# Kernel tuning notes

Hardware: AMD Instinct MI355X
Metric: run time of the kernel (lower is better)

Reference implementation:

```python
import jax, jax.numpy as jnp
import numpy as np

N_NODES = 100000
N_EDGES = 1600000
IN_DIM = 64
OUT_DIM = 64


def setup_inputs() -> dict:
    key = jax.random.key(0)
    k1, k2, k3, k4, k5, k6 = jax.random.split(key, 6)
    # xavier-uniform-ish scales for the linear weights (gain=1.414)
    fc_bound = 1.414 * np.sqrt(6.0 / (IN_DIM + OUT_DIM))
    at_bound = 1.414 * np.sqrt(6.0 / (OUT_DIM + 1))
    return {
        "h_src": jax.random.normal(k1, (N_NODES, IN_DIM), dtype=jnp.float32),
        "h_dst": jax.random.normal(k2, (N_NODES, IN_DIM), dtype=jnp.float32),
        "W_fc": jax.random.uniform(k3, (OUT_DIM, IN_DIM), dtype=jnp.float32,
                                   minval=-fc_bound, maxval=fc_bound),
        "w_attn": jax.random.uniform(k4, (OUT_DIM,), dtype=jnp.float32,
                                     minval=-at_bound, maxval=at_bound),
        "src": jax.random.randint(k5, (N_EDGES,), 0, N_NODES, dtype=jnp.int64),
        "dst": jnp.sort(jax.random.randint(k6, (N_EDGES,), 0, N_NODES, dtype=jnp.int64)),
    }


def reference(h_src, h_dst, W_fc, w_attn, src, dst):
    # Per-edge feature difference: dst - src  (edge_attention)
    diff_e = h_dst[dst] - h_src[src]                      # [E, in_dim]
    # fc projection (dropout p=0 in eval) then attention score
    d = diff_e @ W_fc.T                                   # [E, out_dim]
    e = jnp.tanh(d @ w_attn)                              # [E]
    # Segment softmax over incoming edges of each destination node
    m = jax.ops.segment_max(e, dst, num_segments=N_NODES)  # [N], -inf for empty
    ex = jnp.exp(e - m[dst])                              # [E]
    s = jax.ops.segment_sum(ex, dst, num_segments=N_NODES)  # [N]
    alpha = ex / s[dst]                                   # [E]
    # Weighted sum aggregation of projected diffs per destination node
    h_diff = jax.ops.segment_sum(alpha[:, None] * d, dst, num_segments=N_NODES)  # [N, out_dim]
    return jax.nn.elu(h_diff)
```

## Files before the change

kernel.cpp:

```cpp
#include <hip/hip_runtime.h>
#include <hip/hip_fp16.h>
#include <math.h>

#define NN 100000
#define NE 1600000
#define DIM 64
#define HST 72

typedef __attribute__((ext_vector_type(8))) __fp16 half8;
typedef __attribute__((ext_vector_type(4))) float f32x4;

__device__ __forceinline__ __half2 u2h2(unsigned u) { __half2 h; __builtin_memcpy(&h, &u, 4); return h; }
__device__ __forceinline__ unsigned h22u(__half2 h) { unsigned u; __builtin_memcpy(&u, &h, 4); return u; }
__device__ __forceinline__ unsigned pk_f16(float a, float b) {
    auto h = __builtin_amdgcn_cvt_pkrtz(a, b);
    unsigned u; __builtin_memcpy(&u, &h, 4); return u;
}

__global__ __launch_bounds__(256) void proj_kernel(
    const float* __restrict__ h_src, const float* __restrict__ h_dst,
    const float* __restrict__ W, const float* __restrict__ w_attn,
    unsigned* __restrict__ p16, float* __restrict__ a_src, float* __restrict__ a_dst) {
    __shared__ __align__(16) unsigned short Hh[64 * HST];
    __shared__ __align__(16) unsigned short Wh[64 * HST];
    __shared__ float was[DIM];

    const int t = threadIdx.x;
    const int row0 = blockIdx.x * 64;

#pragma unroll
    for (int r = 0; r < 4; ++r) {
        int idx = (r * 256 + t) * 4;
        int j = idx >> 6, k = idx & 63;
        float4 v = *(const float4*)(W + idx);
        uint2 pk; pk.x = pk_f16(v.x, v.y); pk.y = pk_f16(v.z, v.w);
        *(uint2*)((char*)Wh + j * (HST * 2) + k * 2) = pk;
    }
    if (t < DIM) was[t] = w_attn[t];

#pragma unroll
    for (int r = 0; r < 4; ++r) {
        int idx = (r * 256 + t) * 4;
        int row = idx >> 6, k = idx & 63;
        int grow = row0 + row;
        const float* hp = (grow < NN) ? h_src + (size_t)grow * DIM
                                      : h_dst + (size_t)(grow - NN) * DIM;
        float4 v = *(const float4*)(hp + k);
        uint2 pk; pk.x = pk_f16(v.x, v.y); pk.y = pk_f16(v.z, v.w);
        *(uint2*)((char*)Hh + row * (HST * 2) + k * 2) = pk;
    }
    __syncthreads();

    const int wv = t >> 6, lane = t & 63;
    const int col = lane & 15, quad = lane >> 4;
    const int m0 = wv * 16;

    const char* Hb = (const char*)Hh + (m0 + col) * (HST * 2) + quad * 16;
    half8 af0 = *(const half8*)(Hb);
    half8 af1 = *(const half8*)(Hb + 64);

    f32x4 c[4];
#pragma unroll
    for (int n = 0; n < 4; ++n) {
        const char* Bb = (const char*)Wh + (n * 16 + col) * (HST * 2) + quad * 16;
        half8 b0 = *(const half8*)(Bb);
        half8 b1 = *(const half8*)(Bb + 64);
        f32x4 acc = {0.f, 0.f, 0.f, 0.f};
        acc = __builtin_amdgcn_mfma_f32_16x16x32_f16(af0, b0, acc, 0, 0, 0);
        acc = __builtin_amdgcn_mfma_f32_16x16x32_f16(af1, b1, acc, 0, 0, 0);
        c[n] = acc;
    }

    float wv4[4];
#pragma unroll
    for (int n = 0; n < 4; ++n) wv4[n] = was[n * 16 + col];
#pragma unroll
    for (int reg = 0; reg < 4; ++reg) {
        float pa = c[0][reg] * wv4[0] + c[1][reg] * wv4[1] +
                   c[2][reg] * wv4[2] + c[3][reg] * wv4[3];
#pragma unroll
        for (int off = 1; off <= 8; off <<= 1) pa += __shfl_xor(pa, off);
        if (col == 0) {
            int grow = row0 + m0 + quad * 4 + reg;
            if (grow < NN) a_src[grow] = pa;
            else a_dst[grow - NN] = pa;
        }
    }

    __syncthreads();
    unsigned* Pd = (unsigned*)Hh;
#pragma unroll
    for (int n = 0; n < 4; ++n) {
#pragma unroll
        for (int reg = 0; reg < 4; ++reg) {
            float other = __shfl_xor(c[n][reg], 1);
            if (!(col & 1)) {
                unsigned pk = pk_f16(c[n][reg], other);
                Pd[(m0 + quad * 4 + reg) * 32 + (n * 16 + col) / 2] = pk;
            }
        }
    }
    __syncthreads();
#pragma unroll
    for (int r = 0; r < 2; ++r) {
        int idx = (r * 256 + t) * 4;
        uint4 v = *(const uint4*)(Pd + idx);
        *(uint4*)(p16 + (size_t)row0 * 32 + idx) = v;
    }
}

__global__ void rowptr_kernel(const int* __restrict__ dst, int* __restrict__ row_ptr) {
    int i = blockIdx.x * blockDim.x + threadIdx.x;
    if (i >= NE) return;
    int d = dst[i];
    int prev = (i == 0) ? -1 : dst[i - 1];
    for (int n = prev + 1; n <= d; ++n) row_ptr[n] = i;
    if (i == NE - 1) {
        for (int n = d + 1; n <= NN; ++n) row_ptr[n] = NE;
    }
}

__global__ __launch_bounds__(256) void agg_kernel(
    const char* __restrict__ p16base,
    const float* __restrict__ a_src, const float* __restrict__ a_dst,
    const int* __restrict__ src, const int* __restrict__ row_ptr,
    float4* __restrict__ out4) {
    __shared__ uint2 buf[4][64];
    const int wv = threadIdx.x >> 6;
    const int lane = threadIdx.x & 63;
    const int g = lane >> 4;
    const int glane = lane & 15;
    const int sub16 = glane >> 3;
    const int chunk = glane & 7;

    const int wid = (blockIdx.x * 4 + wv) * 4 + g;
    if (wid >= NN) return;

    const int beg = row_ptr[wid];
    const int end = row_ptr[wid + 1];
    const bool nonempty = end > beg;

    const float ad = nonempty ? a_dst[wid] : 0.f;
    const char* pbase = p16base + (size_t)chunk * 16;
    uint2* bufw = buf[wv];
    const int gbase = g * 16;

    float sAcc = 0.f;
    __half2 acc[4];
#pragma unroll
    for (int q = 0; q < 4; ++q) acc[q] = u2h2(0u);

    for (int cb = beg; cb < end; cb += 16) {
        int cd = end - cb; if (cd > 16) cd = 16;
        uint2 pk = make_uint2(0u, 0u);
        float w = 0.f;
        if (glane < cd) {
            int sv = src[cb + glane];
            float x = ad - a_src[sv];
            float th = 1.f - 2.f / (__expf(2.f * x) + 1.f);
            w = __expf(th);
            pk.x = pk_f16(w, w);
            pk.y = (unsigned)sv * 128u;
        }
        sAcc += w;
        bufw[lane] = pk;

        for (int j = 0; j < cd; j += 4) {
            uint2 e0 = bufw[gbase + j + sub16];
            uint2 e1 = bufw[gbase + j + 2 + sub16];
            uint4 r0 = *(const uint4*)(pbase + e0.y);
            uint4 r1 = *(const uint4*)(pbase + e1.y);
            __half2 w0 = u2h2(e0.x), w1 = u2h2(e1.x);
            acc[0] = __hfma2(w0, u2h2(r0.x), acc[0]);
            acc[1] = __hfma2(w0, u2h2(r0.y), acc[1]);
            acc[2] = __hfma2(w0, u2h2(r0.z), acc[2]);
            acc[3] = __hfma2(w0, u2h2(r0.w), acc[3]);
            acc[0] = __hfma2(w1, u2h2(r1.x), acc[0]);
            acc[1] = __hfma2(w1, u2h2(r1.y), acc[1]);
            acc[2] = __hfma2(w1, u2h2(r1.z), acc[2]);
            acc[3] = __hfma2(w1, u2h2(r1.w), acc[3]);
        }
    }

#pragma unroll
    for (int off = 1; off <= 8; off <<= 1) sAcc += __shfl_xor(sAcc, off);
#pragma unroll
    for (int q = 0; q < 4; ++q)
        acc[q] = __hadd2(acc[q], u2h2(__shfl_xor(h22u(acc[q]), 8)));

    if (sub16 == 0) {
        const uint4 pdu = *(const uint4*)(p16base + ((size_t)(NN + wid)) * 128 + (size_t)chunk * 16);
        const unsigned pw[4] = {pdu.x, pdu.y, pdu.z, pdu.w};
        const float inv = nonempty ? 1.f / sAcc : 0.f;
        float o[8];
#pragma unroll
        for (int q = 0; q < 4; ++q) {
            float2 pf = __half22float2(u2h2(pw[q]));
            float2 af = __half22float2(acc[q]);
            float h0 = nonempty ? (pf.x - af.x * inv) : 0.f;
            float h1 = nonempty ? (pf.y - af.y * inv) : 0.f;
            o[2 * q]     = h0 > 0.f ? h0 : __expf(h0) - 1.f;
            o[2 * q + 1] = h1 > 0.f ? h1 : __expf(h1) - 1.f;
        }
        const size_t ob = (size_t)wid * 16 + chunk * 2;
        out4[ob]     = make_float4(o[0], o[1], o[2], o[3]);
        out4[ob + 1] = make_float4(o[4], o[5], o[6], o[7]);
    }
}

extern "C" void kernel_launch(void* const* d_in, const int* in_sizes, int n_in,
                              void* d_out, int out_size, void* d_ws, size_t ws_size,
                              hipStream_t stream) {
    const float* h_src = (const float*)d_in[0];
    const float* h_dst = (const float*)d_in[1];
    const float* W     = (const float*)d_in[2];
    const float* w_at  = (const float*)d_in[3];
    const int*   src   = (const int*)d_in[4];
    const int*   dst   = (const int*)d_in[5];

    char* ws = (char*)d_ws;
    unsigned* p16 = (unsigned*)ws;
    float* a_src = (float*)(ws + (size_t)2 * NN * 32 * 4);
    float* a_dst = a_src + NN;
    int* row_ptr = (int*)(a_dst + NN);

    hipLaunchKernelGGL(proj_kernel, dim3((2 * NN) / 64), dim3(256), 0, stream,
                       h_src, h_dst, W, w_at, p16, a_src, a_dst);
    hipLaunchKernelGGL(rowptr_kernel, dim3((NE + 255) / 256), dim3(256), 0, stream,
                       dst, row_ptr);
    hipLaunchKernelGGL(agg_kernel, dim3((NN + 15) / 16), dim3(256), 0, stream,
                       (const char*)p16, a_src, a_dst, src, row_ptr,
                       (float4*)d_out);
}
```

Before: 152.2 us.

## Fuse rowptr into projection launch and unroll full-chunk gather in aggregation

Merges the row-pointer construction into the projection kernel as extra blocks, removing one kernel launch and the serialization between the two independent stages. In the aggregation kernel, empty destination nodes now write zeros and exit early, and the destination projection row is loaded before the edge loop. Full 16-edge chunks use an unrolled path that issues all eight gathers before the FMAs to raise memory-level parallelism, at the cost of more registers.

```diff
diff --git a/kernel.cpp b/kernel.cpp
--- a/kernel.cpp
+++ b/kernel.cpp
@@ -6,6 +6,8 @@
 #define NE 1600000
 #define DIM 64
 #define HST 72
+#define PROJ_BLOCKS ((2 * NN) / 64)
+#define ROWPTR_BLOCKS ((NE + 255) / 256)
 
 typedef __attribute__((ext_vector_type(8))) __fp16 half8;
 typedef __attribute__((ext_vector_type(4))) float f32x4;
@@ -20,12 +22,26 @@
 __global__ __launch_bounds__(256) void proj_kernel(
     const float* __restrict__ h_src, const float* __restrict__ h_dst,
     const float* __restrict__ W, const float* __restrict__ w_attn,
+    const int* __restrict__ dst, int* __restrict__ row_ptr,
     unsigned* __restrict__ p16, float* __restrict__ a_src, float* __restrict__ a_dst) {
     __shared__ __align__(16) unsigned short Hh[64 * HST];
     __shared__ __align__(16) unsigned short Wh[64 * HST];
     __shared__ float was[DIM];
 
     const int t = threadIdx.x;
+
+    if (blockIdx.x >= PROJ_BLOCKS) {
+        int i = (blockIdx.x - PROJ_BLOCKS) * 256 + t;
+        if (i >= NE) return;
+        int d = dst[i];
+        int prev = (i == 0) ? -1 : dst[i - 1];
+        for (int n = prev + 1; n <= d; ++n) row_ptr[n] = i;
+        if (i == NE - 1) {
+            for (int n = d + 1; n <= NN; ++n) row_ptr[n] = NE;
+        }
+        return;
+    }
+
     const int row0 = blockIdx.x * 64;
 
 #pragma unroll
@@ -106,17 +122,6 @@
         int idx = (r * 256 + t) * 4;
         uint4 v = *(const uint4*)(Pd + idx);
         *(uint4*)(p16 + (size_t)row0 * 32 + idx) = v;
-    }
-}
-
-__global__ void rowptr_kernel(const int* __restrict__ dst, int* __restrict__ row_ptr) {
-    int i = blockIdx.x * blockDim.x + threadIdx.x;
-    if (i >= NE) return;
-    int d = dst[i];
-    int prev = (i == 0) ? -1 : dst[i - 1];
-    for (int n = prev + 1; n <= d; ++n) row_ptr[n] = i;
-    if (i == NE - 1) {
-        for (int n = d + 1; n <= NN; ++n) row_ptr[n] = NE;
     }
 }
 
@@ -140,7 +145,18 @@
     const int end = row_ptr[wid + 1];
     const bool nonempty = end > beg;
 
-    const float ad = nonempty ? a_dst[wid] : 0.f;
+    if (!nonempty) {
+        if (sub16 == 0) {
+            const size_t ob = (size_t)wid * 16 + chunk * 2;
+            out4[ob]     = make_float4(0.f, 0.f, 0.f, 0.f);
+            out4[ob + 1] = make_float4(0.f, 0.f, 0.f, 0.f);
+        }
+        return;
+    }
+
+    const uint4 pdu = *(const uint4*)(p16base + ((size_t)(NN + wid)) * 128 + (size_t)chunk * 16);
+
+    const float ad = a_dst[wid];
     const char* pbase = p16base + (size_t)chunk * 16;
     uint2* bufw = buf[wv];
     const int gbase = g * 16;
@@ -165,20 +181,37 @@
         sAcc += w;
         bufw[lane] = pk;
 
-        for (int j = 0; j < cd; j += 4) {
-            uint2 e0 = bufw[gbase + j + sub16];
-            uint2 e1 = bufw[gbase + j + 2 + sub16];
-            uint4 r0 = *(const uint4*)(pbase + e0.y);
-            uint4 r1 = *(const uint4*)(pbase + e1.y);
-            __half2 w0 = u2h2(e0.x), w1 = u2h2(e1.x);
-            acc[0] = __hfma2(w0, u2h2(r0.x), acc[0]);
-            acc[1] = __hfma2(w0, u2h2(r0.y), acc[1]);
-            acc[2] = __hfma2(w0, u2h2(r0.z), acc[2]);
-            acc[3] = __hfma2(w0, u2h2(r0.w), acc[3]);
-            acc[0] = __hfma2(w1, u2h2(r1.x), acc[0]);
-            acc[1] = __hfma2(w1, u2h2(r1.y), acc[1]);
-            acc[2] = __hfma2(w1, u2h2(r1.z), acc[2]);
-            acc[3] = __hfma2(w1, u2h2(r1.w), acc[3]);
+        if (cd == 16) {
+            uint2 e[8];
+#pragma unroll
+            for (int q = 0; q < 8; ++q) e[q] = bufw[gbase + 2 * q + sub16];
+            uint4 r[8];
+#pragma unroll
+            for (int q = 0; q < 8; ++q) r[q] = *(const uint4*)(pbase + e[q].y);
+#pragma unroll
+            for (int q = 0; q < 8; ++q) {
+                __half2 wq = u2h2(e[q].x);
+                acc[0] = __hfma2(wq, u2h2(r[q].x), acc[0]);
+                acc[1] = __hfma2(wq, u2h2(r[q].y), acc[1]);
+                acc[2] = __hfma2(wq, u2h2(r[q].z), acc[2]);
+                acc[3] = __hfma2(wq, u2h2(r[q].w), acc[3]);
+            }
+        } else {
+            for (int j = 0; j < cd; j += 4) {
+                uint2 e0 = bufw[gbase + j + sub16];
+                uint2 e1 = bufw[gbase + j + 2 + sub16];
+                uint4 r0 = *(const uint4*)(pbase + e0.y);
+                uint4 r1 = *(const uint4*)(pbase + e1.y);
+                __half2 w0 = u2h2(e0.x), w1 = u2h2(e1.x);
+                acc[0] = __hfma2(w0, u2h2(r0.x), acc[0]);
+                acc[1] = __hfma2(w0, u2h2(r0.y), acc[1]);
+                acc[2] = __hfma2(w0, u2h2(r0.z), acc[2]);
+                acc[3] = __hfma2(w0, u2h2(r0.w), acc[3]);
+                acc[0] = __hfma2(w1, u2h2(r1.x), acc[0]);
+                acc[1] = __hfma2(w1, u2h2(r1.y), acc[1]);
+                acc[2] = __hfma2(w1, u2h2(r1.z), acc[2]);
+                acc[3] = __hfma2(w1, u2h2(r1.w), acc[3]);
+            }
         }
     }
 
@@ -189,16 +222,15 @@
         acc[q] = __hadd2(acc[q], u2h2(__shfl_xor(h22u(acc[q]), 8)));
 
     if (sub16 == 0) {
-        const uint4 pdu = *(const uint4*)(p16base + ((size_t)(NN + wid)) * 128 + (size_t)chunk * 16);
         const unsigned pw[4] = {pdu.x, pdu.y, pdu.z, pdu.w};
-        const float inv = nonempty ? 1.f / sAcc : 0.f;
+        const float inv = 1.f / sAcc;
         float o[8];
 #pragma unroll
         for (int q = 0; q < 4; ++q) {
             float2 pf = __half22float2(u2h2(pw[q]));
             float2 af = __half22float2(acc[q]);
-            float h0 = nonempty ? (pf.x - af.x * inv) : 0.f;
-            float h1 = nonempty ? (pf.y - af.y * inv) : 0.f;
+            float h0 = pf.x - af.x * inv;
+            float h1 = pf.y - af.y * inv;
             o[2 * q]     = h0 > 0.f ? h0 : __expf(h0) - 1.f;
             o[2 * q + 1] = h1 > 0.f ? h1 : __expf(h1) - 1.f;
         }
@@ -224,10 +256,8 @@
     float* a_dst = a_src + NN;
     int* row_ptr = (int*)(a_dst + NN);
 
-    hipLaunchKernelGGL(proj_kernel, dim3((2 * NN) / 64), dim3(256), 0, stream,
-                       h_src, h_dst, W, w_at, p16, a_src, a_dst);
-    hipLaunchKernelGGL(rowptr_kernel, dim3((NE + 255) / 256), dim3(256), 0, stream,
-                       dst, row_ptr);
+    hipLaunchKernelGGL(proj_kernel, dim3(PROJ_BLOCKS + ROWPTR_BLOCKS), dim3(256), 0, stream,
+                       h_src, h_dst, W, w_at, dst, row_ptr, p16, a_src, a_dst);
     hipLaunchKernelGGL(agg_kernel, dim3((NN + 15) / 16), dim3(256), 0, stream,
                        (const char*)p16, a_src, a_dst, src, row_ptr,
                        (float4*)d_out);
```

Measured after the change: 148.8 us, median of 2. -2.2%, faster.
